# Kernel tuning notes

Hardware: AMD Instinct MI355X
Metric: run time of the kernel (lower is better)

## Reference

```python
import jax, jax.numpy as jnp
import numpy as np

B, CIN, H, W = 64, 1, 64, 64
L = 6            # layer_number -> 2^L = 64 blocks per axis
T = 4            # chebyshev_number
C4 = 4 * T * T   # per-block channel width = 64
WK = H // 2 ** (L - 1)  # first-layer kernel/stride = 2
LEFT = H // 2 ** L      # leftover_x = leftover_y = 1


def setup_inputs() -> dict:
    key = jax.random.key(0)
    ks = jax.random.split(key, 16)
    d = {}
    d["x_real"] = jax.random.normal(ks[0], (B, CIN, H, W), jnp.float32)
    d["x_imag"] = jax.random.normal(ks[1], (B, CIN, H, W), jnp.float32)
    # layer 0: per-input-channel conv, 4 -> 4*C4 channels, kernel=stride=WK
    d["w0"] = jax.random.normal(ks[2], (CIN, 4 * C4, 4, WK, WK), jnp.float32) / float(np.sqrt(4 * WK * WK))
    d["b0"] = jnp.zeros((CIN, 4 * C4), jnp.float32)
    # recursion layers lyr=1..L-1: one conv per (channel, block), C4 -> 4*C4, kernel 2x2 stride 2
    for lyr in range(1, L):
        G = 2 ** lyr
        d["w%d" % lyr] = jax.random.normal(ks[2 + lyr], (CIN, G, G, 4 * C4, C4, 2, 2), jnp.float32) / float(np.sqrt(4 * C4))
        d["b%d" % lyr] = jnp.zeros((CIN, G, G, 4 * C4), jnp.float32)
    # final layer: 1x1 conv per block, C4 -> 4*LEFT*LEFT
    GL = 2 ** L
    d["wf"] = jax.random.normal(ks[10], (CIN, GL, GL, 4 * LEFT * LEFT, C4), jnp.float32) / float(np.sqrt(C4))
    d["bf"] = jnp.zeros((CIN, GL, GL, 4 * LEFT * LEFT), jnp.float32)
    return d


def _forward(x_real, x_imag, w0, b0, wrec, brec, wf, bf):
    # split(): [relu(re), relu(im), relu(-re), relu(-im)] per input channel
    xs = jax.nn.relu(jnp.stack([x_real, x_imag, -x_real, -x_imag], axis=2))  # (B,CIN,4,H,W)
    # layer 0: kernel=stride=WK conv as blocked einsum -> (B,CIN,4*C4,P,P), P = 2^(L-1)
    P = H // WK
    xb = xs.reshape(B, CIN, 4, P, WK, P, WK)
    y = jnp.einsum('bcipkql,coikl->bcopq', xb, w0) + b0[None, :, :, None, None]
    y = jax.nn.relu(y)
    # output channels = 2x2 block grid x C4; layout (B,CIN,gy,gx,C4,S,S)
    G, S = 2, P
    y = y.reshape(B, CIN, G, G, C4, S, S)
    for lyr in range(1, L):
        w, b = wrec[lyr - 1], brec[lyr - 1]
        S2 = S // 2
        # 2x2/stride-2 conv per block as batched einsum
        yb = y.reshape(B, CIN, G, G, C4, S2, 2, S2, 2)
        z = jnp.einsum('bcghipkql,cghoikl->bcghopq', yb, w) + b[None, :, :, :, :, None, None]
        z = jax.nn.relu(z)
        # out channels split into (y_loc,x_loc,C4); child block = (2*gy+y_loc, 2*gx+x_loc)
        z = z.reshape(B, CIN, G, G, 2, 2, C4, S2, S2)
        z = z.transpose(0, 1, 2, 4, 3, 5, 6, 7, 8).reshape(B, CIN, 2 * G, 2 * G, C4, S2, S2)
        y, G, S = z, 2 * G, S2
    # final layer: spatial S == 1, 1x1 conv per block
    yv = y[..., 0, 0]                                     # (B,CIN,GL,GL,C4)
    f = jnp.einsum('bcghi,cghoi->bcgho', yv, wf) + bf[None]
    f = jax.nn.relu(f)
    # out channel o = 4*(ky*LEFT+kx)+comp; pixel = (gy*LEFT+ky, gx*LEFT+kx)
    f = f.reshape(B, CIN, G, G, LEFT, LEFT, 4)
    f = f.transpose(0, 1, 2, 4, 3, 5, 6).reshape(B, CIN, H, W, 4)
    # joint(): real = comp0 - comp2, then scale by 1/(H*W)
    return (f[..., 0] - f[..., 2]) / (H * W)


def reference(x_real, x_imag, w0, b0, w1, b1, w2, b2, w3, b3, w4, b4, w5, b5, wf, bf):
    return _forward(x_real, x_imag, w0, b0, (w1, w2, w3, w4, w5), (b1, b2, b3, b4, b5), wf, bf)
```

## Files before the change

kernel.cpp:

```cpp
#include <hip/hip_runtime.h>
#include <cstddef>


typedef unsigned int  u32;
typedef unsigned short u16;
typedef __attribute__((ext_vector_type(8))) short bf16x8;
typedef __attribute__((ext_vector_type(4))) float f32x4;

#define PLANE 16777216

__device__ inline u16 bf16_rn(float x) {
    u32 u = __builtin_bit_cast(u32, x);
    u32 r = (u + 0x7FFFu + ((u >> 16) & 1u)) >> 16;
    return (u16)r;
}
__device__ inline float bf16_to_f(u16 h) {
    u32 u = ((u32)h) << 16;
    return __builtin_bit_cast(float, u);
}
__device__ inline u32 pack_split(float v) {
    const u16 h = bf16_rn(v);
    const u16 l = bf16_rn(v - bf16_to_f(h));
    return (u32)h | ((u32)l << 16);
}
__device__ inline void bar_lds() {
    asm volatile("s_waitcnt lgkmcnt(0)\n\ts_barrier" ::: "memory");
}

__global__ __launch_bounds__(256)
void layer0_kernel(const float* __restrict__ xr, const float* __restrict__ xi,
                   const float* __restrict__ w0, const float* __restrict__ b0,
                   u32* __restrict__ A1) {
    __shared__ float w0s[128][16];
    __shared__ float b0s[128];
    const int og  = blockIdx.y;
    const int tid = threadIdx.x;
    {
        const int row = tid >> 1, half = tid & 1;
        const float4 wa = *(const float4*)(w0 + (og * 128 + row) * 16 + half * 8);
        const float4 wb = *(const float4*)(w0 + (og * 128 + row) * 16 + half * 8 + 4);
        *(float4*)&w0s[row][half * 8]     = wa;
        *(float4*)&w0s[row][half * 8 + 4] = wb;
        if (tid < 128) b0s[tid] = b0[og * 128 + tid];
    }
    __syncthreads();

    const int n = blockIdx.x * 256 + tid;
    const int b = n >> 10, p = (n >> 5) & 31, q = n & 31;
    float xs[16];
#pragma unroll
    for (int k = 0; k < 2; ++k) {
        const float2 vr = *(const float2*)(xr + b * 4096 + (2 * p + k) * 64 + 2 * q);
        const float2 vi = *(const float2*)(xi + b * 4096 + (2 * p + k) * 64 + 2 * q);
        xs[0  + k * 2 + 0] = fmaxf(vr.x, 0.f);  xs[0  + k * 2 + 1] = fmaxf(vr.y, 0.f);
        xs[4  + k * 2 + 0] = fmaxf(vi.x, 0.f);  xs[4  + k * 2 + 1] = fmaxf(vi.y, 0.f);
        xs[8  + k * 2 + 0] = fmaxf(-vr.x, 0.f); xs[8  + k * 2 + 1] = fmaxf(-vr.y, 0.f);
        xs[12 + k * 2 + 0] = fmaxf(-vi.x, 0.f); xs[12 + k * 2 + 1] = fmaxf(-vi.y, 0.f);
    }
    const int kp = p & 1, lp = q & 1, pp = p >> 1, qp = q >> 1;
    const size_t pixoff = (size_t)(b * 256 + pp * 16 + qp);
#pragma unroll
    for (int j = 0; j < 128; ++j) {
        float acc = b0s[j];
#pragma unroll
        for (int e = 0; e < 16; ++e) acc = fmaf(xs[e], w0s[j][e], acc);
        acc = fmaxf(acc, 0.f);
        const int o = og * 128 + j;
        const int gy = o >> 7, gx = (o >> 6) & 1, c = o & 63;
        const size_t flat = (size_t)((((gy * 2 + gx) * 64 + c) * 2 + kp) * 2 + lp) * (64 * 256)
                          + pixoff;
        A1[flat] = pack_split(acc);
    }
}

template<int NT>
__global__ __launch_bounds__(256, 2)
void rec_mfma_kernel(const u32* __restrict__ Yg, const float* __restrict__ Wf,
                     const float* __restrict__ bias, u32* __restrict__ Aout,
                     const int lgG, const int lgS2) {
    constexpr int NF  = NT / 16;
    constexpr int LD  = 40;
    constexpr int NCP = NT / 2;
    constexpr int RPT = 32 / (256 / NCP);

    __shared__ u16 Yhi_s[NT * LD];
    __shared__ u16 Ylo_s[NT * LD];

    const int G  = 1 << lgG;
    const int S2 = 1 << lgS2;
    const int Nb = 64 << (2 * lgS2);

    int bid, nt;
    const int nBid = G * G, NTILES = gridDim.x;
    if (nBid >= 8) {
        const int h = blockIdx.z * NTILES + blockIdx.x;
        const int xcd = h & 7, j = h >> 3, per = nBid >> 3;
        bid = xcd * per + j / NTILES;
        nt  = j % NTILES;
    } else { bid = blockIdx.z; nt = blockIdx.x; }

    const size_t wbase = (size_t)bid * 65536;
    const u32* Yblk = Yg + (size_t)bid * 256 * (size_t)Nb + (size_t)nt * NT;

    const int tid = threadIdx.x, wave = tid >> 6, lane = tid & 63;
    const int l16 = lane & 15, lk = lane >> 4;
    const int cp = tid % NCP, rg = tid / NCP;
    const int col0 = cp * 2, trow = rg * RPT;

    f32x4 acc[4][NF];
#pragma unroll
    for (int m = 0; m < 4; ++m)
#pragma unroll
        for (int n = 0; n < NF; ++n)
            acc[m][n] = (f32x4){0.f, 0.f, 0.f, 0.f};

    uint2  yreg[2][RPT];
    float4 wv[8];
    bf16x8 wh[4], wl[4];
    u32 yhw[2][RPT / 2], ylw[2][RPT / 2];

    auto loadY = [&](int ybuf, int k0) {
#pragma unroll
        for (int r = 0; r < RPT; ++r)
            yreg[ybuf][r] = *(const uint2*)(Yblk + (size_t)(k0 + trow + r) * Nb + col0);
    };
    auto loadWf32 = [&](int k0) {
#pragma unroll
        for (int m = 0; m < 4; ++m) {
            const float* p = Wf + wbase + (size_t)(wave * 64 + m * 16 + l16) * 256 + k0 + lk * 8;
            wv[2 * m]     = *(const float4*)p;
            wv[2 * m + 1] = *(const float4*)(p + 4);
        }
    };
    auto convW = [&]() {
#pragma unroll
        for (int m = 0; m < 4; ++m) {
            union { float4 f4[2]; u32 w[8]; } in;
            in.f4[0] = wv[2 * m];
            in.f4[1] = wv[2 * m + 1];
            union { u32 w[4]; bf16x8 v; } H, L;
#pragma unroll
            for (int j = 0; j < 4; ++j) {
                const u32 u0 = in.w[2 * j], u1 = in.w[2 * j + 1];
                const float x0 = __builtin_bit_cast(float, u0);
                const float x1 = __builtin_bit_cast(float, u1);
                const float h0 = __builtin_bit_cast(float, u0 & 0xFFFF0000u);
                const float h1 = __builtin_bit_cast(float, u1 & 0xFFFF0000u);
                const u32 l0 = __builtin_bit_cast(u32, x0 - h0);
                const u32 l1 = __builtin_bit_cast(u32, x1 - h1);
                H.w[j] = (u0 >> 16) | (u1 & 0xFFFF0000u);
                L.w[j] = (l0 >> 16) | (l1 & 0xFFFF0000u);
            }
            wh[m] = H.v;
            wl[m] = L.v;
        }
    };
    auto prepY = [&](int ybuf) {
#pragma unroll
        for (int c = 0; c < 2; ++c)
#pragma unroll
            for (int j2 = 0; j2 < RPT / 2; ++j2) {
                const u32 a = c ? yreg[ybuf][2 * j2].y     : yreg[ybuf][2 * j2].x;
                const u32 b = c ? yreg[ybuf][2 * j2 + 1].y : yreg[ybuf][2 * j2 + 1].x;
                yhw[c][j2] = (a & 0xFFFFu) | (b << 16);
                ylw[c][j2] = (a >> 16)     | (b & 0xFFFF0000u);
            }
    };
    auto stageY = [&]() {
#pragma unroll
        for (int c = 0; c < 2; ++c) {
            if constexpr (RPT == 8) {
                *(uint4*)&Yhi_s[(col0 + c) * LD + trow] = make_uint4(yhw[c][0], yhw[c][1], yhw[c][2], yhw[c][3]);
                *(uint4*)&Ylo_s[(col0 + c) * LD + trow] = make_uint4(ylw[c][0], ylw[c][1], ylw[c][2], ylw[c][3]);
            } else {
                *(uint2*)&Yhi_s[(col0 + c) * LD + trow] = make_uint2(yhw[c][0], yhw[c][1]);
                *(uint2*)&Ylo_s[(col0 + c) * LD + trow] = make_uint2(ylw[c][0], ylw[c][1]);
            }
        }
    };

    loadY(0, 0); loadY(1, 32);

#pragma unroll
    for (int it = 0; it < 8; ++it) {
        const int k0 = it * 32;
        const int cur = it & 1;
        loadWf32(k0);
        prepY(cur);
        bar_lds();
        stageY();
        bar_lds();
        if (it + 2 < 8) loadY(cur, k0 + 64);
        convW();
        __builtin_amdgcn_s_setprio(1);
#pragma unroll
        for (int n = 0; n < NF; ++n) {
            const int ccol = n * 16 + l16;
            const bf16x8 bhi = *(const bf16x8*)&Yhi_s[ccol * LD + 8 * lk];
            const bf16x8 blo = *(const bf16x8*)&Ylo_s[ccol * LD + 8 * lk];
#pragma unroll
            for (int m = 0; m < 4; ++m)
                acc[m][n] = __builtin_amdgcn_mfma_f32_16x16x32_bf16(wh[m], bhi, acc[m][n], 0, 0, 0);
#pragma unroll
            for (int m = 0; m < 4; ++m)
                acc[m][n] = __builtin_amdgcn_mfma_f32_16x16x32_bf16(wh[m], blo, acc[m][n], 0, 0, 0);
#pragma unroll
            for (int m = 0; m < 4; ++m)
                acc[m][n] = __builtin_amdgcn_mfma_f32_16x16x32_bf16(wl[m], bhi, acc[m][n], 0, 0, 0);
        }
        __builtin_amdgcn_s_setprio(0);
    }

    const int gy = bid >> lgG, gx = bid & (G - 1);
    const int NS2 = S2 >> 1;
#pragma unroll
    for (int m = 0; m < 4; ++m) {
#pragma unroll
        for (int r = 0; r < 4; ++r) {
            const int oc = wave * 64 + m * 16 + lk * 4 + r;
            const float bi = bias[(size_t)bid * 256 + oc];
            const int yl = oc >> 7, xl = (oc >> 6) & 1, cch = oc & 63;
            const int cy = 2 * gy + yl, cx = 2 * gx + xl;
            const size_t base = (size_t)((cy * (2 * G) + cx) * 64 + cch);
#pragma unroll
            for (int n = 0; n < NF; ++n) {
                const float v = fmaxf(acc[m][n][r] + bi, 0.f);
                const int ng = nt * NT + n * 16 + l16;
                const int b   = ng >> (2 * lgS2);
                const int rem = ng & ((1 << (2 * lgS2)) - 1);
                const int p = rem >> lgS2, q = rem & (S2 - 1);
                const size_t flat = ((base * 2 + (p & 1)) * 2 + (q & 1)) * (size_t)(64 * NS2 * NS2)
                                  + (size_t)(b * NS2 * NS2 + (p >> 1) * NS2 + (q >> 1));
                Aout[flat] = pack_split(v);
            }
        }
    }
}

__global__ __launch_bounds__(256, 2)
void rec45_final_kernel(const u32* __restrict__ Yg, const float* __restrict__ W4,
                        const float* __restrict__ b4, const float* __restrict__ W5,
                        const float* __restrict__ b5, const float* __restrict__ wf,
                        const float* __restrict__ bff, float* __restrict__ out) {
    constexpr int LDW = 72;
    __shared__ u16 Whi_w[64 * LDW];
    __shared__ u16 Wlo_w[64 * LDW];

    const int h = blockIdx.x;
    const int parent = ((h >> 5) << 3) | (h & 7);
    const int child  = (h >> 3) & 3;
    const int pgy = parent >> 4, pgx = parent & 15;
    const int cy = 2 * pgy + (child >> 1), cx = 2 * pgx + (child & 1);
    const int bid5 = cy * 32 + cx;
    const int ocbase = child * 64;

    const u32* Yblk  = Yg + (size_t)parent * 65536;
    const float* W4s = W4 + (size_t)parent * 65536 + (size_t)ocbase * 256;
    const float* W5b = W5 + (size_t)bid5 * 65536;

    const int tid = threadIdx.x, wave = tid >> 6, lane = tid & 63;
    const int l16 = lane & 15, lk = lane >> 4;

    f32x4 acc1[4][4];
#pragma unroll
    for (int m = 0; m < 4; ++m)
#pragma unroll
        for (int n = 0; n < 4; ++n)
            acc1[m][n] = (f32x4){0.f, 0.f, 0.f, 0.f};

    u32    yf[2][4][8];
    float4 wv[2][8];
    bf16x8 wh[4], wl[4];

    auto loadY = [&](int buf, int k0) {
#pragma unroll
        for (int n = 0; n < 4; ++n)
#pragma unroll
            for (int j = 0; j < 8; ++j)
                yf[buf][n][j] = Yblk[(size_t)(k0 + 8 * lk + j) * 256 + wave * 64 + n * 16 + l16];
    };
    auto loadW4 = [&](int buf, int k0) {
#pragma unroll
        for (int m = 0; m < 4; ++m) {
            const float* p = W4s + (size_t)(m * 16 + l16) * 256 + k0 + lk * 8;
            wv[buf][2 * m]     = *(const float4*)p;
            wv[buf][2 * m + 1] = *(const float4*)(p + 4);
        }
    };
    auto loadW5 = [&](int buf, int t) {
#pragma unroll
        for (int m = 0; m < 4; ++m) {
            const float* p = W5b + (size_t)(wave * 64 + m * 16 + l16) * 256 + t * 32 + lk * 8;
            wv[buf][2 * m]     = *(const float4*)p;
            wv[buf][2 * m + 1] = *(const float4*)(p + 4);
        }
    };
    auto convW = [&](int buf) {
#pragma unroll
        for (int m = 0; m < 4; ++m) {
            union { float4 f4[2]; u32 w[8]; } in;
            in.f4[0] = wv[buf][2 * m];
            in.f4[1] = wv[buf][2 * m + 1];
            union { u32 w[4]; bf16x8 v; } H, L;
#pragma unroll
            for (int j = 0; j < 4; ++j) {
                const u32 u0 = in.w[2 * j], u1 = in.w[2 * j + 1];
                const float x0 = __builtin_bit_cast(float, u0);
                const float x1 = __builtin_bit_cast(float, u1);
                const float h0 = __builtin_bit_cast(float, u0 & 0xFFFF0000u);
                const float h1 = __builtin_bit_cast(float, u1 & 0xFFFF0000u);
                const u32 l0 = __builtin_bit_cast(u32, x0 - h0);
                const u32 l1 = __builtin_bit_cast(u32, x1 - h1);
                H.w[j] = (u0 >> 16) | (u1 & 0xFFFF0000u);
                L.w[j] = (l0 >> 16) | (l1 & 0xFFFF0000u);
            }
            wh[m] = H.v;
            wl[m] = L.v;
        }
    };

    loadY(0, 0); loadW4(0, 0); loadY(1, 32); loadW4(1, 32);
#pragma unroll
    for (int it = 0; it < 8; ++it) {
        const int cur = it & 1;
        convW(cur);
        __builtin_amdgcn_s_setprio(1);
#pragma unroll
        for (int n = 0; n < 4; ++n) {
            union { u32 w[4]; bf16x8 v; } BH, BL;
#pragma unroll
            for (int j = 0; j < 4; ++j) {
                const u32 y0 = yf[cur][n][2 * j], y1 = yf[cur][n][2 * j + 1];
                BH.w[j] = (y0 & 0xFFFFu) | (y1 << 16);
                BL.w[j] = (y0 >> 16)     | (y1 & 0xFFFF0000u);
            }
#pragma unroll
            for (int m = 0; m < 4; ++m)
                acc1[m][n] = __builtin_amdgcn_mfma_f32_16x16x32_bf16(wh[m], BH.v, acc1[m][n], 0, 0, 0);
#pragma unroll
            for (int m = 0; m < 4; ++m)
                acc1[m][n] = __builtin_amdgcn_mfma_f32_16x16x32_bf16(wh[m], BL.v, acc1[m][n], 0, 0, 0);
#pragma unroll
            for (int m = 0; m < 4; ++m)
                acc1[m][n] = __builtin_amdgcn_mfma_f32_16x16x32_bf16(wl[m], BH.v, acc1[m][n], 0, 0, 0);
        }
        __builtin_amdgcn_s_setprio(0);
        if (it + 2 < 8) { loadY(cur, 32 * it + 64); loadW4(cur, 32 * it + 64); }
    }

    f32x4 acc2[4][4];
#pragma unroll
    for (int m = 0; m < 4; ++m)
#pragma unroll
        for (int n = 0; n < 4; ++n)
            acc2[m][n] = (f32x4){0.f, 0.f, 0.f, 0.f};

    float b4v[4][4];
#pragma unroll
    for (int kw = 0; kw < 4; ++kw)
#pragma unroll
        for (int r = 0; r < 4; ++r)
            b4v[kw][r] = b4[(size_t)parent * 256 + ocbase + kw * 16 + lk * 4 + r];

    loadW5(0, 0); loadW5(1, 1);

#pragma unroll
    for (int kw = 0; kw < 4; ++kw) {
#pragma unroll
        for (int n = 0; n < 4; ++n) {
            const int colg = wave * 64 + n * 16 + l16;
            const int b_ = colg >> 2, par = colg & 3;
#pragma unroll
            for (int r = 0; r < 4; ++r) {
                const float v = fmaxf(acc1[kw][n][r] + b4v[kw][r], 0.f);
                const int k_ = lk * 16 + r * 4 + par;
                const u16 hh = bf16_rn(v);
                Whi_w[b_ * LDW + k_] = hh;
                Wlo_w[b_ * LDW + k_] = bf16_rn(v - bf16_to_f(hh));
            }
        }
        bar_lds();
#pragma unroll
        for (int kc = 0; kc < 2; ++kc) {
            const int t = kw * 2 + kc;
            const int cur = t & 1;
            convW(cur);
            __builtin_amdgcn_s_setprio(1);
#pragma unroll
            for (int n = 0; n < 4; ++n) {
                const int b_ = n * 16 + l16;
                const bf16x8 bhi = *(const bf16x8*)&Whi_w[b_ * LDW + kc * 32 + 8 * lk];
                const bf16x8 blo = *(const bf16x8*)&Wlo_w[b_ * LDW + kc * 32 + 8 * lk];
#pragma unroll
                for (int m = 0; m < 4; ++m)
                    acc2[m][n] = __builtin_amdgcn_mfma_f32_16x16x32_bf16(wh[m], bhi, acc2[m][n], 0, 0, 0);
#pragma unroll
                for (int m = 0; m < 4; ++m)
                    acc2[m][n] = __builtin_amdgcn_mfma_f32_16x16x32_bf16(wh[m], blo, acc2[m][n], 0, 0, 0);
#pragma unroll
                for (int m = 0; m < 4; ++m)
                    acc2[m][n] = __builtin_amdgcn_mfma_f32_16x16x32_bf16(wl[m], bhi, acc2[m][n], 0, 0, 0);
            }
            __builtin_amdgcn_s_setprio(0);
            if (t + 2 < 8) loadW5(cur, t + 2);
        }
        bar_lds();
    }

    const int fy = 2 * cy + (wave >> 1), fx = 2 * cx + (wave & 1);
    const int blk = fy * 64 + fx;
    float wf0v[4][4], wf2v[4][4], biv[4][4];
#pragma unroll
    for (int m = 0; m < 4; ++m)
#pragma unroll
        for (int r = 0; r < 4; ++r) {
            const int cch = m * 16 + lk * 4 + r;
            wf0v[m][r] = wf[(size_t)blk * 256 + cch];
            wf2v[m][r] = wf[(size_t)blk * 256 + 128 + cch];
            biv[m][r]  = b5[(size_t)bid5 * 256 + wave * 64 + cch];
        }
    const float bf0 = bff[blk * 4 + 0], bf2 = bff[blk * 4 + 2];
#pragma unroll
    for (int n = 0; n < 4; ++n) {
        float a0 = 0.f, a2 = 0.f;
#pragma unroll
        for (int m = 0; m < 4; ++m)
#pragma unroll
            for (int r = 0; r < 4; ++r) {
                const float y = fmaxf(acc2[m][n][r] + biv[m][r], 0.f);
                a0 = fmaf(y, wf0v[m][r], a0);
                a2 = fmaf(y, wf2v[m][r], a2);
            }
        a0 += __shfl_xor(a0, 16); a0 += __shfl_xor(a0, 32);
        a2 += __shfl_xor(a2, 16); a2 += __shfl_xor(a2, 32);
        if (lk == n) {
            const float o0 = fmaxf(a0 + bf0, 0.f);
            const float o2 = fmaxf(a2 + bf2, 0.f);
            out[(size_t)(n * 16 + l16) * 4096 + blk] = (o0 - o2) * (1.0f / 4096.0f);
        }
    }
}

extern "C" void kernel_launch(void* const* d_in, const int* in_sizes, int n_in,
                              void* d_out, int out_size, void* d_ws, size_t ws_size,
                              hipStream_t stream) {
    (void)in_sizes; (void)n_in; (void)out_size; (void)ws_size;

    const float* xr = (const float*)d_in[0];
    const float* xi = (const float*)d_in[1];
    const float* w0 = (const float*)d_in[2];
    const float* b0 = (const float*)d_in[3];
    const float* wrec[5] = { (const float*)d_in[4],  (const float*)d_in[6],
                             (const float*)d_in[8],  (const float*)d_in[10],
                             (const float*)d_in[12] };
    const float* brec[5] = { (const float*)d_in[5],  (const float*)d_in[7],
                             (const float*)d_in[9],  (const float*)d_in[11],
                             (const float*)d_in[13] };
    const float* wf = (const float*)d_in[14];
    const float* bf = (const float*)d_in[15];
    float* out = (float*)d_out;

    u32* bufA = (u32*)d_ws;
    u32* bufB = bufA + (size_t)PLANE;

    layer0_kernel<<<dim3(256, 2), 256, 0, stream>>>(xr, xi, w0, b0, bufA);

    rec_mfma_kernel<128><<<dim3(128, 1, 4), 256, 0, stream>>>(
        bufA, wrec[0], brec[0], bufB, 1, 4);
    rec_mfma_kernel<128><<<dim3(32, 1, 16), 256, 0, stream>>>(
        bufB, wrec[1], brec[1], bufA, 2, 3);
    rec_mfma_kernel<128><<<dim3(8, 1, 64), 256, 0, stream>>>(
        bufA, wrec[2], brec[2], bufB, 3, 2);
    rec45_final_kernel<<<1024, 256, 0, stream>>>(
        bufB, wrec[3], brec[3], wrec[4], brec[4], wf, bf, out);
}
```

Before: 263.2 us.

## Fuse recursion layers 2 and 3 into one kernel via LDS handoff

Result: no change. 267.3 us (+1.6%).

```diff
diff --git a/kernel.cpp b/kernel.cpp
--- a/kernel.cpp
+++ b/kernel.cpp
@@ -238,6 +238,202 @@
 }
 
 __global__ __launch_bounds__(256, 2)
+void rec23_kernel(const u32* __restrict__ Yg, const float* __restrict__ W2,
+                  const float* __restrict__ b2, const float* __restrict__ W3,
+                  const float* __restrict__ b3, u32* __restrict__ Aout) {
+    constexpr int LDW = 72;
+    __shared__ u16 Whi_w[64 * LDW];
+    __shared__ u16 Wlo_w[64 * LDW];
+
+    const int h = blockIdx.x;
+    const int parent = ((h >> 5) << 3) | (h & 7);
+    const int child  = (h >> 3) & 3;
+    const int block2 = parent >> 4;
+    const int nt     = parent & 15;
+    const int p2y = block2 >> 2, p2x = block2 & 3;
+    const int cy = 2 * p2y + (child >> 1), cx = 2 * p2x + (child & 1);
+    const int bid3 = cy * 8 + cx;
+    const int ocb = child * 64;
+
+    const u32* Yblk  = Yg + (size_t)block2 * 256 * 4096 + (size_t)nt * 256;
+    const float* W2s = W2 + (size_t)block2 * 65536 + (size_t)ocb * 256;
+    const float* W3b = W3 + (size_t)bid3 * 65536;
+
+    const int tid = threadIdx.x, wave = tid >> 6, lane = tid & 63;
+    const int l16 = lane & 15, lk = lane >> 4;
+
+    f32x4 acc1[4][4];
+#pragma unroll
+    for (int m = 0; m < 4; ++m)
+#pragma unroll
+        for (int n = 0; n < 4; ++n)
+            acc1[m][n] = (f32x4){0.f, 0.f, 0.f, 0.f};
+
+    u32    yf[2][4][8];
+    float4 wv[2][8];
+    bf16x8 wh[4], wl[4];
+
+    auto loadY = [&](int buf, int k0) {
+#pragma unroll
+        for (int n = 0; n < 4; ++n)
+#pragma unroll
+            for (int j = 0; j < 8; ++j)
+                yf[buf][n][j] = Yblk[(size_t)(k0 + 8 * lk + j) * 4096 + wave * 64 + n * 16 + l16];
+    };
+    auto loadW2 = [&](int buf, int k0) {
+#pragma unroll
+        for (int m = 0; m < 4; ++m) {
+            const float* p = W2s + (size_t)(m * 16 + l16) * 256 + k0 + lk * 8;
+            wv[buf][2 * m]     = *(const float4*)p;
+            wv[buf][2 * m + 1] = *(const float4*)(p + 4);
+        }
+    };
+    auto loadW3 = [&](int buf, int t) {
+#pragma unroll
+        for (int m = 0; m < 4; ++m) {
+            const float* p = W3b + (size_t)(wave * 64 + m * 16 + l16) * 256 + t * 32 + lk * 8;
+            wv[buf][2 * m]     = *(const float4*)p;
+            wv[buf][2 * m + 1] = *(const float4*)(p + 4);
+        }
+    };
+    auto convW = [&](int buf) {
+#pragma unroll
+        for (int m = 0; m < 4; ++m) {
+            union { float4 f4[2]; u32 w[8]; } in;
+            in.f4[0] = wv[buf][2 * m];
+            in.f4[1] = wv[buf][2 * m + 1];
+            union { u32 w[4]; bf16x8 v; } H, L;
+#pragma unroll
+            for (int j = 0; j < 4; ++j) {
+                const u32 u0 = in.w[2 * j], u1 = in.w[2 * j + 1];
+                const float x0 = __builtin_bit_cast(float, u0);
+                const float x1 = __builtin_bit_cast(float, u1);
+                const float h0 = __builtin_bit_cast(float, u0 & 0xFFFF0000u);
+                const float h1 = __builtin_bit_cast(float, u1 & 0xFFFF0000u);
+                const u32 l0 = __builtin_bit_cast(u32, x0 - h0);
+                const u32 l1 = __builtin_bit_cast(u32, x1 - h1);
+                H.w[j] = (u0 >> 16) | (u1 & 0xFFFF0000u);
+                L.w[j] = (l0 >> 16) | (l1 & 0xFFFF0000u);
+            }
+            wh[m] = H.v;
+            wl[m] = L.v;
+        }
+    };
+
+    loadY(0, 0); loadW2(0, 0); loadY(1, 32); loadW2(1, 32);
+#pragma unroll
+    for (int it = 0; it < 8; ++it) {
+        const int cur = it & 1;
+        convW(cur);
+        __builtin_amdgcn_s_setprio(1);
+#pragma unroll
+        for (int n = 0; n < 4; ++n) {
+            union { u32 w[4]; bf16x8 v; } BH, BL;
+#pragma unroll
+            for (int j = 0; j < 4; ++j) {
+                const u32 y0 = yf[cur][n][2 * j], y1 = yf[cur][n][2 * j + 1];
+                BH.w[j] = (y0 & 0xFFFFu) | (y1 << 16);
+                BL.w[j] = (y0 >> 16)     | (y1 & 0xFFFF0000u);
+            }
+#pragma unroll
+            for (int m = 0; m < 4; ++m)
+                acc1[m][n] = __builtin_amdgcn_mfma_f32_16x16x32_bf16(wh[m], BH.v, acc1[m][n], 0, 0, 0);
+#pragma unroll
+            for (int m = 0; m < 4; ++m)
+                acc1[m][n] = __builtin_amdgcn_mfma_f32_16x16x32_bf16(wh[m], BL.v, acc1[m][n], 0, 0, 0);
+#pragma unroll
+            for (int m = 0; m < 4; ++m)
+                acc1[m][n] = __builtin_amdgcn_mfma_f32_16x16x32_bf16(wl[m], BH.v, acc1[m][n], 0, 0, 0);
+        }
+        __builtin_amdgcn_s_setprio(0);
+        if (it + 2 < 8) { loadY(cur, 32 * it + 64); loadW2(cur, 32 * it + 64); }
+    }
+
+    f32x4 acc2[4][4];
+#pragma unroll
+    for (int m = 0; m < 4; ++m)
+#pragma unroll
+        for (int n = 0; n < 4; ++n)
+            acc2[m][n] = (f32x4){0.f, 0.f, 0.f, 0.f};
+
+    float b2v[4][4];
+#pragma unroll
+    for (int kw = 0; kw < 4; ++kw)
+#pragma unroll
+        for (int r = 0; r < 4; ++r)
+            b2v[kw][r] = b2[(size_t)block2 * 256 + ocb + kw * 16 + lk * 4 + r];
+
+    loadW3(0, 0); loadW3(1, 1);
+
+#pragma unroll
+    for (int kw = 0; kw < 4; ++kw) {
+        {
+            const int wcol_base = wave * 16 + ((l16 & 7) >> 1);
+            const int kl = ((l16 >> 3) & 1) * 2 + (l16 & 1);
+#pragma unroll
+            for (int n = 0; n < 4; ++n) {
+#pragma unroll
+                for (int r = 0; r < 4; ++r) {
+                    const float v = fmaxf(acc1[kw][n][r] + b2v[kw][r], 0.f);
+                    const int col = wcol_base + n * 4;
+                    const int kloc = (lk * 4 + r) * 4 + kl;
+                    const u16 hh = bf16_rn(v);
+                    Whi_w[col * LDW + kloc] = hh;
+                    Wlo_w[col * LDW + kloc] = bf16_rn(v - bf16_to_f(hh));
+                }
+            }
+        }
+        bar_lds();
+#pragma unroll
+        for (int kc = 0; kc < 2; ++kc) {
+            const int t = kw * 2 + kc;
+            const int cur = t & 1;
+            convW(cur);
+            __builtin_amdgcn_s_setprio(1);
+#pragma unroll
+            for (int n = 0; n < 4; ++n) {
+                const int c_ = n * 16 + l16;
+                const bf16x8 bhi = *(const bf16x8*)&Whi_w[c_ * LDW + kc * 32 + 8 * lk];
+                const bf16x8 blo = *(const bf16x8*)&Wlo_w[c_ * LDW + kc * 32 + 8 * lk];
+#pragma unroll
+                for (int m = 0; m < 4; ++m)
+                    acc2[m][n] = __builtin_amdgcn_mfma_f32_16x16x32_bf16(wh[m], bhi, acc2[m][n], 0, 0, 0);
+#pragma unroll
+                for (int m = 0; m < 4; ++m)
+                    acc2[m][n] = __builtin_amdgcn_mfma_f32_16x16x32_bf16(wh[m], blo, acc2[m][n], 0, 0, 0);
+#pragma unroll
+                for (int m = 0; m < 4; ++m)
+                    acc2[m][n] = __builtin_amdgcn_mfma_f32_16x16x32_bf16(wl[m], bhi, acc2[m][n], 0, 0, 0);
+            }
+            __builtin_amdgcn_s_setprio(0);
+            if (t + 2 < 8) loadW3(cur, t + 2);
+        }
+        bar_lds();
+    }
+
+#pragma unroll
+    for (int m = 0; m < 4; ++m) {
+#pragma unroll
+        for (int r = 0; r < 4; ++r) {
+            const int oc = wave * 64 + m * 16 + lk * 4 + r;
+            const float bi = b3[(size_t)bid3 * 256 + oc];
+            const int yl = oc >> 7, xl = (oc >> 6) & 1, cch = oc & 63;
+            const int cy4 = 2 * cy + yl, cx4 = 2 * cx + xl;
+            const size_t base = (size_t)((cy4 * 16 + cx4) * 64 + cch);
+            const int u3 = l16 >> 2, v3 = l16 & 3;
+#pragma unroll
+            for (int nf = 0; nf < 4; ++nf) {
+                const float v = fmaxf(acc2[m][nf][r] + bi, 0.f);
+                const int b = 4 * nt + nf;
+                const size_t flat = ((base * 2 + (u3 & 1)) * 2 + (v3 & 1)) * (size_t)256
+                                  + (size_t)(b * 4 + (u3 >> 1) * 2 + (v3 >> 1));
+                Aout[flat] = pack_split(v);
+            }
+        }
+    }
+}
+
+__global__ __launch_bounds__(256, 2)
 void rec45_final_kernel(const u32* __restrict__ Yg, const float* __restrict__ W4,
                         const float* __restrict__ b4, const float* __restrict__ W5,
                         const float* __restrict__ b5, const float* __restrict__ wf,
@@ -467,10 +663,8 @@
 
     rec_mfma_kernel<128><<<dim3(128, 1, 4), 256, 0, stream>>>(
         bufA, wrec[0], brec[0], bufB, 1, 4);
-    rec_mfma_kernel<128><<<dim3(32, 1, 16), 256, 0, stream>>>(
-        bufB, wrec[1], brec[1], bufA, 2, 3);
-    rec_mfma_kernel<128><<<dim3(8, 1, 64), 256, 0, stream>>>(
-        bufA, wrec[2], brec[2], bufB, 3, 2);
+    rec23_kernel<<<1024, 256, 0, stream>>>(
+        bufB, wrec[1], brec[1], wrec[2], brec[2], bufA);
     rec45_final_kernel<<<1024, 256, 0, stream>>>(
-        bufB, wrec[3], brec[3], wrec[4], brec[4], wf, bf, out);
-}
+        bufA, wrec[3], brec[3], wrec[4], brec[4], wf, bf, out);
+}
```
